# Performance work log

Measured on AMD Instinct MI355X. Metric: run time of the kernel, lower is better.

Reference implementation:

```python
import jax, jax.numpy as jnp
import numpy as np

EPS = 1e-6
KH, KW = 3, 3
SH, SW = 1, 1


def _unfold(x, kh, kw, sh, sw):
    # x: [N, C, H, W] -> patches [N, C, kh*kw, L], L = ox*oy (torch.nn.Unfold layout)
    N, C, H, W = x.shape
    ox = (H - kh) // sh + 1
    oy = (W - kw) // sw + 1
    pats = [x[:, :, i:i + sh * ox:sh, j:j + sw * oy:sw]
            for i in range(kh) for j in range(kw)]
    p = jnp.stack(pats, axis=2)  # [N, C, K, ox, oy]
    return p.reshape(N, C, kh * kw, ox * oy), ox, oy


def setup_inputs() -> dict:
    key = jax.random.key(0)
    kx, k1, k2 = jax.random.split(key, 3)
    x = jax.random.uniform(kx, (32, 2, 64, 64, 64), dtype=jnp.float32)
    w1 = jax.random.uniform(k1, (64, KH * KW), dtype=jnp.float32)
    w2 = jax.random.uniform(k2, (128, 64), dtype=jnp.float32)
    return {"x": x, "w1": w1, "w2": w2}


def reference(x, w1, w2):
    B = x.shape[0]
    out_ch = w2.shape[0]
    xr = x[:, 0]  # rotation plane [B, C, H, W]
    xa = x[:, 1]  # magnitude plane

    pr, ox, oy = _unfold(xr, KH, KW, SH, SW)  # [B, C, K, L]
    pa, _, _ = _unfold(xa, KH, KW, SH, SW)

    # weightNormalize1: squared weights normalized by GLOBAL sum (rot branch)
    w1_glob = w1 ** 2 / jnp.sum(w1 ** 2)
    w2_glob = w2 ** 2 / jnp.sum(w2 ** 2)
    # weightNormalize (drop_prob=0): squared weights normalized PER ROW (abs branch)
    w1_row = w1 ** 2 / jnp.sum(w1 ** 2, axis=1, keepdims=True)
    w2_row = w2 ** 2 / jnp.sum(w2 ** 2, axis=1, keepdims=True)

    # rotation branch: two weighted contractions
    rot = jnp.einsum('bckl,ck->bcl', pr, w1_glob)          # [B, C, L]
    out_rot = jnp.einsum('bcl,oc->bol', rot, w2_glob)      # [B, O, L]
    out_rot = out_rot.reshape(B, 1, out_ch, ox, oy)

    # magnitude branch: log -> weighted contractions -> exp
    la = jnp.log(pa + EPS)                                  # [B, C, K, L]
    a1 = jnp.einsum('bckl,ck->bcl', la, w1_row)             # [B, C, L]
    out_abs = jnp.exp(jnp.einsum('bcl,oc->bol', a1, w2_row))
    out_abs = out_abs.reshape(B, 1, out_ch, ox, oy)

    return jnp.concatenate([out_rot, out_abs], axis=1)  # [B, 2, O, ox, oy]
```

## Files before the change

kernel.cpp:

```cpp
#include <hip/hip_runtime.h>
#include <cstdint>
#include <cstddef>

#define EPSF 1e-6f

typedef __attribute__((ext_vector_type(4))) float f32x4;
typedef __attribute__((ext_vector_type(8))) short s16x8;
typedef union { s16x8 v; unsigned u[4]; } s16x8u;

static __device__ __forceinline__ void pack2(float a, float b, unsigned& H, unsigned& L) {
    unsigned h, l;
    asm("v_cvt_pk_bf16_f32 %0, %1, %2" : "=v"(h) : "v"(a), "v"(b));
    float ra = a - __uint_as_float(h << 16);
    float rb = b - __uint_as_float(h & 0xffff0000u);
    asm("v_cvt_pk_bf16_f32 %0, %1, %2" : "=v"(l) : "v"(ra), "v"(rb));
    H = h; L = l;
}
static __device__ __forceinline__ unsigned packH(float a, float b) {
    unsigned h;
    asm("v_cvt_pk_bf16_f32 %0, %1, %2" : "=v"(h) : "v"(a), "v"(b));
    return h;
}


__global__ __launch_bounds__(256) void prep(const float* __restrict__ w1,
                                            const float* __restrict__ w2,
                                            float* __restrict__ ws) {
    __shared__ float s1row[64];
    __shared__ float red[4];
    __shared__ float rs8[8];
    const int t = threadIdx.x;
    const int lane = t & 63;
    const int wv = t >> 6;
    const int gid = blockIdx.x * 256 + t;

    float s = 0.f;
    #pragma unroll
    for (int i = 0; i < 32; ++i) { float v = w2[t + 256 * i]; s += v * v; }
    #pragma unroll
    for (int d = 32; d > 0; d >>= 1) s += __shfl_xor(s, d);
    if (lane == 0) red[wv] = s;

    if (t < 64) {
        float rs = 0.f;
        #pragma unroll
        for (int k = 0; k < 9; ++k) { float v = w1[t * 9 + k]; rs += v * v; }
        s1row[t] = rs;
    }

    if (blockIdx.x < 16) {
        const int r8 = t >> 5;
        const int e = t & 31;
        const int row = blockIdx.x * 8 + r8;
        float v0 = w2[row * 64 + e];
        float v1 = w2[row * 64 + 32 + e];
        float rr = v0 * v0 + v1 * v1;
        #pragma unroll
        for (int d = 16; d > 0; d >>= 1) rr += __shfl_down(rr, d);
        if (e == 0) rs8[r8] = rr;
    }
    __syncthreads();

    const float t2 = red[0] + red[1] + red[2] + red[3];
    float a = s1row[lane];
    #pragma unroll
    for (int d = 32; d > 0; d >>= 1) a += __shfl_xor(a, d);
    const float t1 = a;

    unsigned* wsu = (unsigned*)ws;
    if (gid < 4096) {
        const int row = gid >> 5;
        const int cp = gid & 31;
        float v0 = w2[row * 64 + 2 * cp];
        float v1 = w2[row * 64 + 2 * cp + 1];
        float q0 = v0 * v0, q1 = v1 * v1;
        const float rs = rs8[t >> 5];
        unsigned H, L;
        pack2(q0 / t2, q1 / t2, H, L);
        wsu[1152 + row * 32 + cp] = H;
        wsu[5248 + row * 32 + cp] = L;
        pack2(q0 / rs, q1 / rs, H, L);
        wsu[9344 + row * 32 + cp] = H;
        wsu[13440 + row * 32 + cp] = L;
    } else if (gid < 4672) {
        const int i = gid - 4096;
        const int c = i / 9;
        const int k = i - c * 9;
        float v = w1[i];
        float q = v * v;
        ws[c * 9 + k] = q / t1;
        ws[576 + c * 9 + k] = q / s1row[c];
    }
}

__global__ __launch_bounds__(512, 8) void conv_fused(const float* __restrict__ x,
                                                     const float* __restrict__ ws,
                                                     float* __restrict__ out) {
    const int b = blockIdx.x;
    const int branch = blockIdx.y;
    const int hg = blockIdx.z;
    const int h0 = hg * 2;
    const int t = threadIdx.x;
    const int lane = t & 63;
    const int w = __builtin_amdgcn_readfirstlane(t >> 6);
    const int lm = lane & 15;
    const int q = lane >> 4;
    const bool dual = (branch != 0);

    __shared__ unsigned rotH[128 * 33];
    __shared__ unsigned rotL[128 * 33];

    const float* __restrict__ w1n = ws + branch * 576;
    const unsigned* __restrict__ wsu = (const unsigned*)ws;
    const unsigned* __restrict__ w2H = wsu + 1152 + branch * 8192;
    const unsigned* __restrict__ w2L = w2H + 4096;
    const float* __restrict__ xb = x + (size_t)(b * 2 + branch) * (64 * 4096);

    const int woc = (w & 3) * 32;
    const int half = w >> 2;
    const int cpair = w * 4 + q;
    const int c0 = 2 * cpair;

    {
        const float* xp0 = xb + c0 * 4096 + h0 * 64 + 4 * lm;
        float4 va[4], vb[4];
        #pragma unroll
        for (int r = 0; r < 4; ++r) va[r] = *(const float4*)(xp0 + r * 64);
        #pragma unroll
        for (int r = 0; r < 4; ++r) vb[r] = *(const float4*)(xp0 + 4096 + r * 64);

        const float* wc0 = w1n + c0 * 9;
        float pa[2][4], pb[2][4];

        if (dual) {
            #pragma unroll
            for (int r = 0; r < 4; ++r) {
                va[r].x = __logf(va[r].x + EPSF); va[r].y = __logf(va[r].y + EPSF);
                va[r].z = __logf(va[r].z + EPSF); va[r].w = __logf(va[r].w + EPSF);
            }
        }
        {
            float sax[4], say[4];
            #pragma unroll
            for (int r = 0; r < 4; ++r) {
                sax[r] = __shfl_down(va[r].x, 1); say[r] = __shfl_down(va[r].y, 1);
            }
            #pragma unroll
            for (int row = 0; row < 2; ++row) {
                #pragma unroll
                for (int rr = 0; rr < 3; ++rr) {
                    const float4 u = va[row + rr];
                    const float ux1 = sax[row + rr], uy1 = say[row + rr];
                    const float t0 = wc0[rr * 3], t1_ = wc0[rr * 3 + 1], t2_ = wc0[rr * 3 + 2];
                    if (rr == 0) {
                        pa[row][0] = u.x * t0 + u.y * t1_ + u.z * t2_;
                        pa[row][1] = u.y * t0 + u.z * t1_ + u.w * t2_;
                        pa[row][2] = u.z * t0 + u.w * t1_ + ux1 * t2_;
                        pa[row][3] = u.w * t0 + ux1 * t1_ + uy1 * t2_;
                    } else {
                        pa[row][0] += u.x * t0 + u.y * t1_ + u.z * t2_;
                        pa[row][1] += u.y * t0 + u.z * t1_ + u.w * t2_;
                        pa[row][2] += u.z * t0 + u.w * t1_ + ux1 * t2_;
                        pa[row][3] += u.w * t0 + ux1 * t1_ + uy1 * t2_;
                    }
                }
            }
        }

        if (dual) {
            #pragma unroll
            for (int r = 0; r < 4; ++r) {
                vb[r].x = __logf(vb[r].x + EPSF); vb[r].y = __logf(vb[r].y + EPSF);
                vb[r].z = __logf(vb[r].z + EPSF); vb[r].w = __logf(vb[r].w + EPSF);
            }
        }
        {
            const float* wc1 = wc0 + 9;
            float sbx[4], sby[4];
            #pragma unroll
            for (int r = 0; r < 4; ++r) {
                sbx[r] = __shfl_down(vb[r].x, 1); sby[r] = __shfl_down(vb[r].y, 1);
            }
            #pragma unroll
            for (int row = 0; row < 2; ++row) {
                #pragma unroll
                for (int rr = 0; rr < 3; ++rr) {
                    const float4 u = vb[row + rr];
                    const float ux1 = sbx[row + rr], uy1 = sby[row + rr];
                    const float t0 = wc1[rr * 3], t1_ = wc1[rr * 3 + 1], t2_ = wc1[rr * 3 + 2];
                    if (rr == 0) {
                        pb[row][0] = u.x * t0 + u.y * t1_ + u.z * t2_;
                        pb[row][1] = u.y * t0 + u.z * t1_ + u.w * t2_;
                        pb[row][2] = u.z * t0 + u.w * t1_ + ux1 * t2_;
                        pb[row][3] = u.w * t0 + ux1 * t1_ + uy1 * t2_;
                    } else {
                        pb[row][0] += u.x * t0 + u.y * t1_ + u.z * t2_;
                        pb[row][1] += u.y * t0 + u.z * t1_ + u.w * t2_;
                        pb[row][2] += u.z * t0 + u.w * t1_ + ux1 * t2_;
                        pb[row][3] += u.w * t0 + ux1 * t1_ + uy1 * t2_;
                    }
                }
            }
        }

        #pragma unroll
        for (int row = 0; row < 2; ++row) {
            #pragma unroll
            for (int ii = 0; ii < 4; ++ii) {
                const int pxl = row * 64 + 4 * lm + ii;
                if (dual) {
                    unsigned H, L;
                    pack2(pa[row][ii], pb[row][ii], H, L);
                    rotH[pxl * 33 + cpair] = H;
                    rotL[pxl * 33 + cpair] = L;
                } else {
                    rotH[pxl * 33 + cpair] = packH(pa[row][ii], pb[row][ii]);
                }
            }
        }
    }

    s16x8u aH[2][2];
    #pragma unroll
    for (int mt = 0; mt < 2; ++mt) {
        #pragma unroll
        for (int kk = 0; kk < 2; ++kk) {
            const int off = (woc + mt * 16 + lm) * 32 + kk * 16 + q * 4;
            #pragma unroll
            for (int j = 0; j < 4; ++j) aH[mt][kk].u[j] = w2H[off + j];
        }
    }
    __syncthreads();

    #pragma unroll
    for (int mt = 0; mt < 2; ++mt) {
        f32x4 acc[4];
        #pragma unroll
        for (int nt = 0; nt < 4; ++nt) acc[nt] = (f32x4){0.f, 0.f, 0.f, 0.f};

        if (dual) {
            s16x8u aL[2];
            #pragma unroll
            for (int kk = 0; kk < 2; ++kk) {
                const int off = (woc + mt * 16 + lm) * 32 + kk * 16 + q * 4;
                #pragma unroll
                for (int j = 0; j < 4; ++j) aL[kk].u[j] = w2L[off + j];
            }
            __builtin_amdgcn_s_setprio(1);
            #pragma unroll
            for (int nt = 0; nt < 4; ++nt) {
                #pragma unroll
                for (int kk = 0; kk < 2; ++kk) {
                    const int idx = (half * 64 + nt * 16 + lm) * 33 + kk * 16 + q * 4;
                    s16x8u bH, bL;
                    #pragma unroll
                    for (int j = 0; j < 4; ++j) bH.u[j] = rotH[idx + j];
                    #pragma unroll
                    for (int j = 0; j < 4; ++j) bL.u[j] = rotL[idx + j];
                    acc[nt] = __builtin_amdgcn_mfma_f32_16x16x32_bf16(aH[mt][kk].v, bH.v, acc[nt], 0, 0, 0);
                    acc[nt] = __builtin_amdgcn_mfma_f32_16x16x32_bf16(aH[mt][kk].v, bL.v, acc[nt], 0, 0, 0);
                    acc[nt] = __builtin_amdgcn_mfma_f32_16x16x32_bf16(aL[kk].v, bH.v, acc[nt], 0, 0, 0);
                }
            }
            __builtin_amdgcn_s_setprio(0);
        } else {
            __builtin_amdgcn_s_setprio(1);
            #pragma unroll
            for (int nt = 0; nt < 4; ++nt) {
                #pragma unroll
                for (int kk = 0; kk < 2; ++kk) {
                    const int idx = (half * 64 + nt * 16 + lm) * 33 + kk * 16 + q * 4;
                    s16x8u bH;
                    #pragma unroll
                    for (int j = 0; j < 4; ++j) bH.u[j] = rotH[idx + j];
                    acc[nt] = __builtin_amdgcn_mfma_f32_16x16x32_bf16(aH[mt][kk].v, bH.v, acc[nt], 0, 0, 0);
                }
            }
            __builtin_amdgcn_s_setprio(0);
        }

        const int oc0 = woc + mt * 16 + q * 4;
        #pragma unroll
        for (int nt = 0; nt < 4; ++nt) {
            const int col = nt * 16 + lm;
            if (col < 62) {
                const size_t base =
                    ((size_t)((b * 2 + branch) * 128 + oc0)) * 3844 +
                    (size_t)(h0 + half) * 62 + col;
                #pragma unroll
                for (int r = 0; r < 4; ++r) {
                    float v = acc[nt][r];
                    if (dual) v = __expf(v);
                    out[base + (size_t)r * 3844] = v;
                }
            }
        }
    }
}

extern "C" void kernel_launch(void* const* d_in, const int* in_sizes, int n_in,
                              void* d_out, int out_size, void* d_ws, size_t ws_size,
                              hipStream_t stream) {
    const float* x  = (const float*)d_in[0];
    const float* w1 = (const float*)d_in[1];
    const float* w2 = (const float*)d_in[2];
    float* out = (float*)d_out;
    float* ws  = (float*)d_ws;

    prep<<<19, 256, 0, stream>>>(w1, w2, ws);

    dim3 grid(32, 2, 31);
    conv_fused<<<grid, 512, 0, stream>>>(x, ws, out);
}
```

Measured before the change: 213.4 us.

## Process one output row per block and give each wave a 16-channel tile

Each block now handles a single output row instead of two, which doubles the grid and halves the shared-memory staging buffers. Each of the 8 waves owns 16 output channels across all 64 pixels, replacing the old 32-channel by half-row split. Right-edge neighbours now come from extra float2 global loads instead of lane shuffles, and the w2 fragments are loaded before the convolution math so their latency overlaps it. Per-block work and register pressure drop and parallelism rises, but each input row is reread by three blocks instead of being shared across two rows, and launch bounds are lowered to 4.

```diff
diff --git a/kernel.cpp b/kernel.cpp
--- a/kernel.cpp
+++ b/kernel.cpp
@@ -93,13 +93,12 @@
     }
 }
 
-__global__ __launch_bounds__(512, 8) void conv_fused(const float* __restrict__ x,
+__global__ __launch_bounds__(512, 4) void conv_fused(const float* __restrict__ x,
                                                      const float* __restrict__ ws,
                                                      float* __restrict__ out) {
     const int b = blockIdx.x;
     const int branch = blockIdx.y;
-    const int hg = blockIdx.z;
-    const int h0 = hg * 2;
+    const int h = blockIdx.z;
     const int t = threadIdx.x;
     const int lane = t & 63;
     const int w = __builtin_amdgcn_readfirstlane(t >> 6);
@@ -107,8 +106,8 @@
     const int q = lane >> 4;
     const bool dual = (branch != 0);
 
-    __shared__ unsigned rotH[128 * 33];
-    __shared__ unsigned rotL[128 * 33];
+    __shared__ unsigned rotH[64 * 33];
+    __shared__ unsigned rotL[64 * 33];
 
     const float* __restrict__ w1n = ws + branch * 576;
     const unsigned* __restrict__ wsu = (const unsigned*)ws;
@@ -116,183 +115,163 @@
     const unsigned* __restrict__ w2L = w2H + 4096;
     const float* __restrict__ xb = x + (size_t)(b * 2 + branch) * (64 * 4096);
 
-    const int woc = (w & 3) * 32;
-    const int half = w >> 2;
     const int cpair = w * 4 + q;
     const int c0 = 2 * cpair;
+    const int oc0 = w * 16;
+
+    const float* xp = xb + c0 * 4096 + h * 64;
+    const int x0 = 4 * lm;
+    const int xe = (lm < 15) ? 4 * lm + 4 : 60;
+
+    float pa[4], pb[4];
+
+    float4 va[3]; float2 ea[3];
+    #pragma unroll
+    for (int r = 0; r < 3; ++r) va[r] = *(const float4*)(xp + r * 64 + x0);
+    #pragma unroll
+    for (int r = 0; r < 3; ++r) ea[r] = *(const float2*)(xp + r * 64 + xe);
+
+    s16x8u aH[2], aL[2];
+    #pragma unroll
+    for (int kk = 0; kk < 2; ++kk) {
+        const int off = (oc0 + lm) * 32 + kk * 16 + q * 4;
+        #pragma unroll
+        for (int j = 0; j < 4; ++j) aH[kk].u[j] = w2H[off + j];
+    }
+    if (dual) {
+        #pragma unroll
+        for (int kk = 0; kk < 2; ++kk) {
+            const int off = (oc0 + lm) * 32 + kk * 16 + q * 4;
+            #pragma unroll
+            for (int j = 0; j < 4; ++j) aL[kk].u[j] = w2L[off + j];
+        }
+    }
+
+    const float* wc0 = w1n + c0 * 9;
+    if (dual) {
+        #pragma unroll
+        for (int r = 0; r < 3; ++r) {
+            va[r].x = __logf(va[r].x + EPSF); va[r].y = __logf(va[r].y + EPSF);
+            va[r].z = __logf(va[r].z + EPSF); va[r].w = __logf(va[r].w + EPSF);
+            ea[r].x = __logf(ea[r].x + EPSF); ea[r].y = __logf(ea[r].y + EPSF);
+        }
+    }
+    #pragma unroll
+    for (int rr = 0; rr < 3; ++rr) {
+        const float4 u = va[rr];
+        const float e0 = ea[rr].x, e1 = ea[rr].y;
+        const float t0 = wc0[rr * 3], t1_ = wc0[rr * 3 + 1], t2_ = wc0[rr * 3 + 2];
+        if (rr == 0) {
+            pa[0] = u.x * t0 + u.y * t1_ + u.z * t2_;
+            pa[1] = u.y * t0 + u.z * t1_ + u.w * t2_;
+            pa[2] = u.z * t0 + u.w * t1_ + e0 * t2_;
+            pa[3] = u.w * t0 + e0 * t1_ + e1 * t2_;
+        } else {
+            pa[0] += u.x * t0 + u.y * t1_ + u.z * t2_;
+            pa[1] += u.y * t0 + u.z * t1_ + u.w * t2_;
+            pa[2] += u.z * t0 + u.w * t1_ + e0 * t2_;
+            pa[3] += u.w * t0 + e0 * t1_ + e1 * t2_;
+        }
+    }
 
     {
-        const float* xp0 = xb + c0 * 4096 + h0 * 64 + 4 * lm;
-        float4 va[4], vb[4];
-        #pragma unroll
-        for (int r = 0; r < 4; ++r) va[r] = *(const float4*)(xp0 + r * 64);
-        #pragma unroll
-        for (int r = 0; r < 4; ++r) vb[r] = *(const float4*)(xp0 + 4096 + r * 64);
-
-        const float* wc0 = w1n + c0 * 9;
-        float pa[2][4], pb[2][4];
-
+        float4 vb[3]; float2 eb[3];
+        #pragma unroll
+        for (int r = 0; r < 3; ++r) vb[r] = *(const float4*)(xp + 4096 + r * 64 + x0);
+        #pragma unroll
+        for (int r = 0; r < 3; ++r) eb[r] = *(const float2*)(xp + 4096 + r * 64 + xe);
+
+        const float* wc1 = wc0 + 9;
         if (dual) {
             #pragma unroll
-            for (int r = 0; r < 4; ++r) {
-                va[r].x = __logf(va[r].x + EPSF); va[r].y = __logf(va[r].y + EPSF);
-                va[r].z = __logf(va[r].z + EPSF); va[r].w = __logf(va[r].w + EPSF);
-            }
-        }
-        {
-            float sax[4], say[4];
-            #pragma unroll
-            for (int r = 0; r < 4; ++r) {
-                sax[r] = __shfl_down(va[r].x, 1); say[r] = __shfl_down(va[r].y, 1);
-            }
-            #pragma unroll
-            for (int row = 0; row < 2; ++row) {
-                #pragma unroll
-                for (int rr = 0; rr < 3; ++rr) {
-                    const float4 u = va[row + rr];
-                    const float ux1 = sax[row + rr], uy1 = say[row + rr];
-                    const float t0 = wc0[rr * 3], t1_ = wc0[rr * 3 + 1], t2_ = wc0[rr * 3 + 2];
-                    if (rr == 0) {
-                        pa[row][0] = u.x * t0 + u.y * t1_ + u.z * t2_;
-                        pa[row][1] = u.y * t0 + u.z * t1_ + u.w * t2_;
-                        pa[row][2] = u.z * t0 + u.w * t1_ + ux1 * t2_;
-                        pa[row][3] = u.w * t0 + ux1 * t1_ + uy1 * t2_;
-                    } else {
-                        pa[row][0] += u.x * t0 + u.y * t1_ + u.z * t2_;
-                        pa[row][1] += u.y * t0 + u.z * t1_ + u.w * t2_;
-                        pa[row][2] += u.z * t0 + u.w * t1_ + ux1 * t2_;
-                        pa[row][3] += u.w * t0 + ux1 * t1_ + uy1 * t2_;
-                    }
-                }
-            }
-        }
-
-        if (dual) {
-            #pragma unroll
-            for (int r = 0; r < 4; ++r) {
+            for (int r = 0; r < 3; ++r) {
                 vb[r].x = __logf(vb[r].x + EPSF); vb[r].y = __logf(vb[r].y + EPSF);
                 vb[r].z = __logf(vb[r].z + EPSF); vb[r].w = __logf(vb[r].w + EPSF);
-            }
-        }
-        {
-            const float* wc1 = wc0 + 9;
-            float sbx[4], sby[4];
+                eb[r].x = __logf(eb[r].x + EPSF); eb[r].y = __logf(eb[r].y + EPSF);
+            }
+        }
+        #pragma unroll
+        for (int rr = 0; rr < 3; ++rr) {
+            const float4 u = vb[rr];
+            const float e0 = eb[rr].x, e1 = eb[rr].y;
+            const float t0 = wc1[rr * 3], t1_ = wc1[rr * 3 + 1], t2_ = wc1[rr * 3 + 2];
+            if (rr == 0) {
+                pb[0] = u.x * t0 + u.y * t1_ + u.z * t2_;
+                pb[1] = u.y * t0 + u.z * t1_ + u.w * t2_;
+                pb[2] = u.z * t0 + u.w * t1_ + e0 * t2_;
+                pb[3] = u.w * t0 + e0 * t1_ + e1 * t2_;
+            } else {
+                pb[0] += u.x * t0 + u.y * t1_ + u.z * t2_;
+                pb[1] += u.y * t0 + u.z * t1_ + u.w * t2_;
+                pb[2] += u.z * t0 + u.w * t1_ + e0 * t2_;
+                pb[3] += u.w * t0 + e0 * t1_ + e1 * t2_;
+            }
+        }
+    }
+
+    #pragma unroll
+    for (int i = 0; i < 4; ++i) {
+        const int px = 4 * lm + i;
+        if (dual) {
+            unsigned H, L;
+            pack2(pa[i], pb[i], H, L);
+            rotH[px * 33 + cpair] = H;
+            rotL[px * 33 + cpair] = L;
+        } else {
+            rotH[px * 33 + cpair] = packH(pa[i], pb[i]);
+        }
+    }
+    __syncthreads();
+
+    f32x4 acc[4];
+    #pragma unroll
+    for (int nt = 0; nt < 4; ++nt) acc[nt] = (f32x4){0.f, 0.f, 0.f, 0.f};
+
+    __builtin_amdgcn_s_setprio(1);
+    if (dual) {
+        #pragma unroll
+        for (int nt = 0; nt < 4; ++nt) {
+            #pragma unroll
+            for (int kk = 0; kk < 2; ++kk) {
+                const int idx = (nt * 16 + lm) * 33 + kk * 16 + q * 4;
+                s16x8u bH, bL;
+                #pragma unroll
+                for (int j = 0; j < 4; ++j) bH.u[j] = rotH[idx + j];
+                #pragma unroll
+                for (int j = 0; j < 4; ++j) bL.u[j] = rotL[idx + j];
+                acc[nt] = __builtin_amdgcn_mfma_f32_16x16x32_bf16(aH[kk].v, bH.v, acc[nt], 0, 0, 0);
+                acc[nt] = __builtin_amdgcn_mfma_f32_16x16x32_bf16(aH[kk].v, bL.v, acc[nt], 0, 0, 0);
+                acc[nt] = __builtin_amdgcn_mfma_f32_16x16x32_bf16(aL[kk].v, bH.v, acc[nt], 0, 0, 0);
+            }
+        }
+    } else {
+        #pragma unroll
+        for (int nt = 0; nt < 4; ++nt) {
+            #pragma unroll
+            for (int kk = 0; kk < 2; ++kk) {
+                const int idx = (nt * 16 + lm) * 33 + kk * 16 + q * 4;
+                s16x8u bH;
+                #pragma unroll
+                for (int j = 0; j < 4; ++j) bH.u[j] = rotH[idx + j];
+                acc[nt] = __builtin_amdgcn_mfma_f32_16x16x32_bf16(aH[kk].v, bH.v, acc[nt], 0, 0, 0);
+            }
+        }
+    }
+    __builtin_amdgcn_s_setprio(0);
+
+    const int ocr = oc0 + q * 4;
+    #pragma unroll
+    for (int nt = 0; nt < 4; ++nt) {
+        const int col = nt * 16 + lm;
+        if (col < 62) {
+            const size_t base =
+                ((size_t)((b * 2 + branch) * 128 + ocr)) * 3844 +
+                (size_t)h * 62 + col;
             #pragma unroll
             for (int r = 0; r < 4; ++r) {
-                sbx[r] = __shfl_down(vb[r].x, 1); sby[r] = __shfl_down(vb[r].y, 1);
-            }
-            #pragma unroll
-            for (int row = 0; row < 2; ++row) {
-                #pragma unroll
-                for (int rr = 0; rr < 3; ++rr) {
-                    const float4 u = vb[row + rr];
-                    const float ux1 = sbx[row + rr], uy1 = sby[row + rr];
-                    const float t0 = wc1[rr * 3], t1_ = wc1[rr * 3 + 1], t2_ = wc1[rr * 3 + 2];
-                    if (rr == 0) {
-                        pb[row][0] = u.x * t0 + u.y * t1_ + u.z * t2_;
-                        pb[row][1] = u.y * t0 + u.z * t1_ + u.w * t2_;
-                        pb[row][2] = u.z * t0 + u.w * t1_ + ux1 * t2_;
-                        pb[row][3] = u.w * t0 + ux1 * t1_ + uy1 * t2_;
-                    } else {
-                        pb[row][0] += u.x * t0 + u.y * t1_ + u.z * t2_;
-                        pb[row][1] += u.y * t0 + u.z * t1_ + u.w * t2_;
-                        pb[row][2] += u.z * t0 + u.w * t1_ + ux1 * t2_;
-                        pb[row][3] += u.w * t0 + ux1 * t1_ + uy1 * t2_;
-                    }
-                }
-            }
-        }
-
-        #pragma unroll
-        for (int row = 0; row < 2; ++row) {
-            #pragma unroll
-            for (int ii = 0; ii < 4; ++ii) {
-                const int pxl = row * 64 + 4 * lm + ii;
-                if (dual) {
-                    unsigned H, L;
-                    pack2(pa[row][ii], pb[row][ii], H, L);
-                    rotH[pxl * 33 + cpair] = H;
-                    rotL[pxl * 33 + cpair] = L;
-                } else {
-                    rotH[pxl * 33 + cpair] = packH(pa[row][ii], pb[row][ii]);
-                }
-            }
-        }
-    }
-
-    s16x8u aH[2][2];
-    #pragma unroll
-    for (int mt = 0; mt < 2; ++mt) {
-        #pragma unroll
-        for (int kk = 0; kk < 2; ++kk) {
-            const int off = (woc + mt * 16 + lm) * 32 + kk * 16 + q * 4;
-            #pragma unroll
-            for (int j = 0; j < 4; ++j) aH[mt][kk].u[j] = w2H[off + j];
-        }
-    }
-    __syncthreads();
-
-    #pragma unroll
-    for (int mt = 0; mt < 2; ++mt) {
-        f32x4 acc[4];
-        #pragma unroll
-        for (int nt = 0; nt < 4; ++nt) acc[nt] = (f32x4){0.f, 0.f, 0.f, 0.f};
-
-        if (dual) {
-            s16x8u aL[2];
-            #pragma unroll
-            for (int kk = 0; kk < 2; ++kk) {
-                const int off = (woc + mt * 16 + lm) * 32 + kk * 16 + q * 4;
-                #pragma unroll
-                for (int j = 0; j < 4; ++j) aL[kk].u[j] = w2L[off + j];
-            }
-            __builtin_amdgcn_s_setprio(1);
-            #pragma unroll
-            for (int nt = 0; nt < 4; ++nt) {
-                #pragma unroll
-                for (int kk = 0; kk < 2; ++kk) {
-                    const int idx = (half * 64 + nt * 16 + lm) * 33 + kk * 16 + q * 4;
-                    s16x8u bH, bL;
-                    #pragma unroll
-                    for (int j = 0; j < 4; ++j) bH.u[j] = rotH[idx + j];
-                    #pragma unroll
-                    for (int j = 0; j < 4; ++j) bL.u[j] = rotL[idx + j];
-                    acc[nt] = __builtin_amdgcn_mfma_f32_16x16x32_bf16(aH[mt][kk].v, bH.v, acc[nt], 0, 0, 0);
-                    acc[nt] = __builtin_amdgcn_mfma_f32_16x16x32_bf16(aH[mt][kk].v, bL.v, acc[nt], 0, 0, 0);
-                    acc[nt] = __builtin_amdgcn_mfma_f32_16x16x32_bf16(aL[kk].v, bH.v, acc[nt], 0, 0, 0);
-                }
-            }
-            __builtin_amdgcn_s_setprio(0);
-        } else {
-            __builtin_amdgcn_s_setprio(1);
-            #pragma unroll
-            for (int nt = 0; nt < 4; ++nt) {
-                #pragma unroll
-                for (int kk = 0; kk < 2; ++kk) {
-                    const int idx = (half * 64 + nt * 16 + lm) * 33 + kk * 16 + q * 4;
-                    s16x8u bH;
-                    #pragma unroll
-                    for (int j = 0; j < 4; ++j) bH.u[j] = rotH[idx + j];
-                    acc[nt] = __builtin_amdgcn_mfma_f32_16x16x32_bf16(aH[mt][kk].v, bH.v, acc[nt], 0, 0, 0);
-                }
-            }
-            __builtin_amdgcn_s_setprio(0);
-        }
-
-        const int oc0 = woc + mt * 16 + q * 4;
-        #pragma unroll
-        for (int nt = 0; nt < 4; ++nt) {
-            const int col = nt * 16 + lm;
-            if (col < 62) {
-                const size_t base =
-                    ((size_t)((b * 2 + branch) * 128 + oc0)) * 3844 +
-                    (size_t)(h0 + half) * 62 + col;
-                #pragma unroll
-                for (int r = 0; r < 4; ++r) {
-                    float v = acc[nt][r];
-                    if (dual) v = __expf(v);
-                    out[base + (size_t)r * 3844] = v;
-                }
+                float v = acc[nt][r];
+                if (dual) v = __expf(v);
+                out[base + (size_t)r * 3844] = v;
             }
         }
     }
@@ -309,6 +288,6 @@
 
     prep<<<19, 256, 0, stream>>>(w1, w2, ws);
 
-    dim3 grid(32, 2, 31);
+    dim3 grid(32, 2, 62);
     conv_fused<<<grid, 512, 0, stream>>>(x, ws, out);
 }
```

Result: no change. 214.1 us (+0.3%).
